# Optimization experiments

Hardware: AMD Instinct MI355X
Metric: run time of the kernel (lower is better)

Reference implementation:

```python
import jax, jax.numpy as jnp
import numpy as np

NF, EF, H, G, T, LAYERS = 133, 14, 300, 200, 12, 3
B, N_PER, PAIRS = 4096, 32, 32
N, E = B * N_PER, B * PAIRS * 2
R1, R2 = 550, 378  # readout dims per config defaults


def setup_inputs() -> dict:
    key = jax.random.key(0)
    ks = jax.random.split(key, 16)
    rng = np.random.default_rng(0)
    # edges within each graph, laid out as reverse pairs: 2i = (u->w), 2i+1 = (w->u)
    u = rng.integers(0, N_PER, size=(B, PAIRS))
    w = (u + 1 + rng.integers(0, N_PER - 1, size=(B, PAIRS))) % N_PER  # w != u
    offs = (np.arange(B) * N_PER)[:, None]
    u, w = u + offs, w + offs
    src = np.stack([u, w], axis=-1).reshape(-1).astype(np.int64)
    dst = np.stack([w, u], axis=-1).reshape(-1).astype(np.int64)
    node_graph = np.repeat(np.arange(B), N_PER).astype(np.int64)

    def lin(k, fin, fout):
        s = (2.0 / (fin + fout)) ** 0.5  # xavier_normal, gain=1
        return jax.random.normal(k, (fin, fout), jnp.float32) * s

    return {
        "v": jax.random.normal(ks[0], (N, NF + 1), jnp.float32),
        "e": jax.random.normal(ks[1], (E, EF + 1), jnp.float32),
        "globals_": jax.random.normal(ks[2], (B, G), jnp.float32),
        "Wi": lin(ks[3], NF + EF, H), "bi": jnp.zeros((H,), jnp.float32),
        "Wm": lin(ks[4], H, H), "bm": jnp.zeros((H,), jnp.float32),
        "Wa": lin(ks[5], NF + H, H), "ba": jnp.zeros((H,), jnp.float32),
        "Wr1": lin(ks[6], G + H, R1), "br1": jnp.zeros((R1,), jnp.float32),
        "Wr2": lin(ks[7], R1, R2), "br2": jnp.zeros((R2,), jnp.float32),
        "Wr3": lin(ks[8], R2, T), "br3": jnp.zeros((T,), jnp.float32),
        "src": jnp.asarray(src), "dst": jnp.asarray(dst),
        "node_graph": jnp.asarray(node_graph),
    }


def reference(v, e, globals_, Wi, bi, Wm, bm, Wa, ba,
              Wr1, br1, Wr2, br2, Wr3, br3, src, dst, node_graph):
    n = v.shape[0]
    b = globals_.shape[0]
    vv = v[:, :NF]          # strip trailing 'r' column
    ee = e[:, :EF]
    # edge init: h_0 = relu(W_i [src_v ; e])
    h0 = jax.nn.relu(jnp.concatenate([vv[src], ee], axis=1) @ Wi + bi)  # [E,H]
    rev = jnp.arange(h0.shape[0]) ^ 1  # reverse-pair edge layout
    h = h0
    for _ in range(LAYERS):
        # non-backtracking line-graph sum: incoming-to-src minus reverse edge
        acc = jax.ops.segment_sum(h, dst, num_segments=n)   # [N,H]
        m_e = acc[src] - h[rev]                             # [E,H]
        h = jax.nn.relu(h0 + m_e @ Wm + bm)                 # dropout p=0
    # reverse-graph copy_e sum => aggregate edges by ORIGINAL src node
    m_v = jax.ops.segment_sum(h, src, num_segments=n)       # [N,H]
    h_v = jax.nn.relu(jnp.concatenate([vv, m_v], axis=1) @ Wa + ba)
    # mean readout per graph
    cnt = jax.ops.segment_sum(jnp.ones((n,), v.dtype), node_graph, num_segments=b)
    out = jax.ops.segment_sum(h_v, node_graph, num_segments=b) / cnt[:, None]
    out = jax.nn.relu(jnp.concatenate([out, globals_], axis=1) @ Wr1 + br1)
    out = jax.nn.relu(out @ Wr2 + br2)
    return out @ Wr3 + br3
```

## Files before the change

### kernel.cpp

```cpp
#include <hip/hip_runtime.h>

typedef __bf16 bf16x8 __attribute__((ext_vector_type(8)));
typedef float f32x4 __attribute__((ext_vector_type(4)));
typedef unsigned short u16;
typedef unsigned int u32;
typedef unsigned long long u64;

#define NF_ 133
#define EF_ 14
#define HD 300
#define KH 320
#define K0 160
#define K2 448
#define NT 19
#define SHP 2432

__device__ __forceinline__ u16 f2bf(float f) {
    union { float f; u32 u; } v; v.f = f;
    u32 r = v.u + 0x7fffu + ((v.u >> 16) & 1u);
    return (u16)(r >> 16);
}
__device__ __forceinline__ float bf2f(u16 h) {
    union { u32 u; float f; } v; v.u = ((u32)h) << 16;
    return v.f;
}

__global__ void prep_w(const float* __restrict__ W, u16* __restrict__ Wt,
                       int K, int N, int KP, int NP, int gap) {
    int idx = blockIdx.x * 256 + threadIdx.x;
    if (idx >= NP * KP) return;
    int n = idx / KP, k = idx - n * KP;
    int kk = k;
    if (gap) kk = (k < 133) ? k : ((k >= 136 && k < 436) ? k - 3 : -1);
    float val = (kk >= 0 && kk < K && n < N) ? W[kk * N + n] : 0.f;
    Wt[idx] = f2bf(val);
}

__global__ void prep_glob(const float* __restrict__ glob, u16* __restrict__ Ar1) {
    int idx = blockIdx.x * 256 + threadIdx.x;
    if (idx >= 4096 * 212) return;
    int g = idx / 212, c = 300 + (idx - g * 212);
    float val = (c < 500) ? glob[g * 200 + (c - 300)] : 0.f;
    Ar1[g * 512 + c] = f2bf(val);
}

__global__ __launch_bounds__(512, 2) void gnn_mega(
    const float* __restrict__ vf, const float* __restrict__ ef,
    const int* __restrict__ src, const int* __restrict__ dst,
    const u16* __restrict__ WiT, const u16* __restrict__ WmT, const u16* __restrict__ WaT,
    const float* __restrict__ bi, const float* __restrict__ bm, const float* __restrict__ ba,
    u16* __restrict__ Ar1)
{
    __shared__ u16 sm[64 * KH];
    __shared__ u16 shT[8 * SHP];
    __shared__ u64 s_amask[32];
    __shared__ u64 s_smask[32];
    __shared__ int s_src[64];
    __shared__ unsigned char s_src8[64];

    const int g = blockIdx.x;
    const int tid = threadIdx.x;
    const int wave = tid >> 6;
    const int lane = tid & 63;
    const int lm = lane & 15;
    const int q = lane >> 4;

    if (tid < 64) {
        int sv = src[g * 64 + tid] - g * 32;
        int dv = dst[g * 64 + tid] - g * 32;
        s_src[tid] = sv;
        s_src8[tid] = (unsigned char)sv;
        #pragma unroll 1
        for (int n = 0; n < 32; ++n) {
            u64 bmA = __ballot(dv == n);
            u64 bmS = __ballot(sv == n);
            if (tid == 0) { s_amask[n] = bmA; s_smask[n] = bmS; }
        }
    }
    for (int i = tid; i < 9728; i += 512) ((u32*)shT)[i] = 0u;
    if (tid < 512) ((u32*)sm)[9728 + tid] = 0u;
    __syncthreads();

    for (int idx = tid; idx < 64 * K0; idx += 512) {
        int ed = idx / K0, c = idx - ed * K0;
        float val = 0.f;
        if (c < NF_) val = vf[(size_t)(g * 32 + s_src[ed]) * (NF_ + 1) + c];
        else if (c < NF_ + EF_) val = ef[(size_t)(g * 64 + ed) * (EF_ + 1) + (c - NF_)];
        sm[((c >> 3) << 9) + (ed << 3) + (c & 7)] = f2bf(val);
    }
    __syncthreads();

    u64 h0p[3][4];
    float bmv[3];
    {
        f32x4 acc[3][4];
        #pragma unroll
        for (int t = 0; t < 3; ++t)
            #pragma unroll
            for (int mt = 0; mt < 4; ++mt) acc[t][mt] = (f32x4){0.f, 0.f, 0.f, 0.f};
        #pragma unroll
        for (int ks = 0; ks < 5; ++ks) {
            bf16x8 af[4];
            #pragma unroll
            for (int mt = 0; mt < 4; ++mt)
                af[mt] = *(const bf16x8*)&sm[((ks * 4 + q) << 9) + ((mt * 16 + lm) << 3)];
            #pragma unroll
            for (int t = 0; t < 3; ++t) {
                int j = 8 * t + wave;
                if (j < NT) {
                    bf16x8 bfr = *(const bf16x8*)&WiT[(j * 16 + lm) * K0 + ks * 32 + q * 8];
                    #pragma unroll
                    for (int mt = 0; mt < 4; ++mt)
                        acc[t][mt] = __builtin_amdgcn_mfma_f32_16x16x32_bf16(af[mt], bfr, acc[t][mt], 0, 0, 0);
                }
            }
        }
        #pragma unroll
        for (int t = 0; t < 3; ++t) {
            int j = 8 * t + wave;
            int n = j * 16 + lm;
            bool ok = (j < NT) && (n < HD);
            float bv = ok ? bi[n] : 0.f;
            bmv[t] = ok ? bm[n] : 0.f;
            #pragma unroll
            for (int mt = 0; mt < 4; ++mt) {
                u64 w = 0;
                #pragma unroll
                for (int r = 0; r < 4; ++r) {
                    float hv = acc[t][mt][r] + bv;
                    hv = hv > 0.f ? hv : 0.f;
                    w |= ((u64)f2bf(hv)) << (16 * r);
                }
                h0p[t][mt] = w;
                if (ok) *(u64*)&shT[(mt * 2 + (q >> 1)) * SHP + n * 8 + (q & 1) * 4] = w;
            }
        }
    }

    for (int layer = 0; layer < 3; ++layer) {
        __syncthreads();
        {
            u64 am[4];
            #pragma unroll
            for (int mt = 0; mt < 4; ++mt) {
                int e = mt * 16 + lm;
                am[mt] = s_amask[s_src8[e]] & ~(1ull << (e ^ 1));
            }
            bf16x8 bfrag[2][4];
            #pragma unroll
            for (int ks = 0; ks < 2; ++ks) {
                int kb = ks * 32 + q * 8;
                #pragma unroll
                for (int mt = 0; mt < 4; ++mt) {
                    union { u32 w[4]; bf16x8 v; } fb;
                    #pragma unroll
                    for (int jj = 0; jj < 4; ++jj) {
                        u32 lo = (u32)((am[mt] >> (kb + 2 * jj)) & 1ull) * 0x3F80u;
                        u32 hi = (u32)((am[mt] >> (kb + 2 * jj + 1)) & 1ull) * 0x3F80u;
                        fb.w[jj] = lo | (hi << 16);
                    }
                    bfrag[ks][mt] = fb.v;
                }
            }
            #pragma unroll
            for (int t = 0; t < 3; ++t) {
                int j = 8 * t + wave;
                if (j < NT) {
                    f32x4 mac[4];
                    #pragma unroll
                    for (int mt = 0; mt < 4; ++mt) mac[mt] = (f32x4){0.f, 0.f, 0.f, 0.f};
                    #pragma unroll
                    for (int ks = 0; ks < 2; ++ks) {
                        bf16x8 af = *(const bf16x8*)&shT[(ks * 4 + q) * SHP + (j * 16 + lm) * 8];
                        #pragma unroll
                        for (int mt = 0; mt < 4; ++mt)
                            mac[mt] = __builtin_amdgcn_mfma_f32_16x16x32_bf16(af, bfrag[ks][mt], mac[mt], 0, 0, 0);
                    }
                    #pragma unroll
                    for (int mt = 0; mt < 4; ++mt) {
                        u64 w = 0;
                        #pragma unroll
                        for (int r = 0; r < 4; ++r) w |= ((u64)f2bf(mac[mt][r])) << (16 * r);
                        *(u64*)&sm[(j * 2 + (q >> 1)) * 512 + (mt * 16 + lm) * 8 + (q & 1) * 4] = w;
                    }
                }
            }
        }
        __syncthreads();
        {
            f32x4 acc[3][4];
            #pragma unroll
            for (int t = 0; t < 3; ++t)
                #pragma unroll
                for (int mt = 0; mt < 4; ++mt) acc[t][mt] = (f32x4){0.f, 0.f, 0.f, 0.f};
            #pragma unroll
            for (int ks = 0; ks < 10; ++ks) {
                bf16x8 af[4];
                #pragma unroll
                for (int mt = 0; mt < 4; ++mt)
                    af[mt] = *(const bf16x8*)&sm[((ks * 4 + q) << 9) + ((mt * 16 + lm) << 3)];
                #pragma unroll
                for (int t = 0; t < 3; ++t) {
                    int j = 8 * t + wave;
                    if (j < NT) {
                        bf16x8 bfr = *(const bf16x8*)&WmT[(j * 16 + lm) * KH + ks * 32 + q * 8];
                        #pragma unroll
                        for (int mt = 0; mt < 4; ++mt)
                            acc[t][mt] = __builtin_amdgcn_mfma_f32_16x16x32_bf16(af[mt], bfr, acc[t][mt], 0, 0, 0);
                    }
                }
            }
            #pragma unroll
            for (int t = 0; t < 3; ++t) {
                int j = 8 * t + wave;
                int n = j * 16 + lm;
                bool ok = (j < NT) && (n < HD);
                #pragma unroll
                for (int mt = 0; mt < 4; ++mt) {
                    u64 w = 0;
                    #pragma unroll
                    for (int r = 0; r < 4; ++r) {
                        float h0v = bf2f((u16)(h0p[t][mt] >> (16 * r)));
                        float hv = h0v + acc[t][mt][r] + bmv[t];
                        hv = hv > 0.f ? hv : 0.f;
                        w |= ((u64)f2bf(hv)) << (16 * r);
                    }
                    if (ok) *(u64*)&shT[(mt * 2 + (q >> 1)) * SHP + n * 8 + (q & 1) * 4] = w;
                }
            }
        }
    }
    __syncthreads();

    for (int idx = tid; idx < 32 * K2; idx += 512) {
        int n = idx / K2, c = idx - n * K2;
        float val = (c < NF_) ? vf[(size_t)(g * 32 + n) * (NF_ + 1) + c] : 0.f;
        sm[((c >> 3) << 8) + (n << 3) + (c & 7)] = f2bf(val);
    }
    __syncthreads();

    {
        bf16x8 sfrag[2][2];
        #pragma unroll
        for (int ks = 0; ks < 2; ++ks) {
            int kb = ks * 32 + q * 8;
            #pragma unroll
            for (int mt = 0; mt < 2; ++mt) {
                u64 msk = s_smask[mt * 16 + lm];
                union { u32 w[4]; bf16x8 v; } fb;
                #pragma unroll
                for (int jj = 0; jj < 4; ++jj) {
                    u32 lo = (u32)((msk >> (kb + 2 * jj)) & 1ull) * 0x3F80u;
                    u32 hi = (u32)((msk >> (kb + 2 * jj + 1)) & 1ull) * 0x3F80u;
                    fb.w[jj] = lo | (hi << 16);
                }
                sfrag[ks][mt] = fb.v;
            }
        }
        #pragma unroll
        for (int t = 0; t < 3; ++t) {
            int j = 8 * t + wave;
            if (j < NT) {
                f32x4 vacc[2];
                #pragma unroll
                for (int mt = 0; mt < 2; ++mt) vacc[mt] = (f32x4){0.f, 0.f, 0.f, 0.f};
                #pragma unroll
                for (int ks = 0; ks < 2; ++ks) {
                    bf16x8 af = *(const bf16x8*)&shT[(ks * 4 + q) * SHP + (j * 16 + lm) * 8];
                    #pragma unroll
                    for (int mt = 0; mt < 2; ++mt)
                        vacc[mt] = __builtin_amdgcn_mfma_f32_16x16x32_bf16(af, sfrag[ks][mt], vacc[mt], 0, 0, 0);
                }
                #pragma unroll
                for (int mt = 0; mt < 2; ++mt) {
                    u64 w = 0;
                    #pragma unroll
                    for (int r = 0; r < 4; ++r) w |= ((u64)f2bf(vacc[mt][r])) << (16 * r);
                    *(u64*)&sm[(17 + j * 2 + (q >> 1)) * 256 + (mt * 16 + lm) * 8 + (q & 1) * 4] = w;
                }
            }
        }
    }
    __syncthreads();

    {
        f32x4 acc2[3][2];
        #pragma unroll
        for (int t = 0; t < 3; ++t)
            #pragma unroll
            for (int mt = 0; mt < 2; ++mt) acc2[t][mt] = (f32x4){0.f, 0.f, 0.f, 0.f};
        #pragma unroll
        for (int ks = 0; ks < 14; ++ks) {
            bf16x8 af[2];
            #pragma unroll
            for (int mt = 0; mt < 2; ++mt)
                af[mt] = *(const bf16x8*)&sm[((ks * 4 + q) << 8) + ((mt * 16 + lm) << 3)];
            #pragma unroll
            for (int t = 0; t < 3; ++t) {
                int j = 8 * t + wave;
                if (j < NT) {
                    bf16x8 bfr = *(const bf16x8*)&WaT[(j * 16 + lm) * K2 + ks * 32 + q * 8];
                    #pragma unroll
                    for (int mt = 0; mt < 2; ++mt)
                        acc2[t][mt] = __builtin_amdgcn_mfma_f32_16x16x32_bf16(af[mt], bfr, acc2[t][mt], 0, 0, 0);
                }
            }
        }
        #pragma unroll
        for (int t = 0; t < 3; ++t) {
            int j = 8 * t + wave;
            int n = j * 16 + lm;
            bool ok = (j < NT) && (n < HD);
            float bav = ok ? ba[n] : 0.f;
            float s = 0.f;
            #pragma unroll
            for (int mt = 0; mt < 2; ++mt)
                #pragma unroll
                for (int r = 0; r < 4; ++r) {
                    float hv = acc2[t][mt][r] + bav;
                    s += (hv > 0.f ? hv : 0.f);
                }
            s += __shfl_xor(s, 16);
            s += __shfl_xor(s, 32);
            if (ok && q == 0) Ar1[g * 512 + n] = f2bf(s * 0.03125f);
        }
    }
}

template<int RELU, int OUTBF16>
__global__ __launch_bounds__(256, 4) void gemm_ro(
    const u16* __restrict__ A, const u16* __restrict__ Bt, const float* __restrict__ bias,
    const int KP, const int Nreal, const int outPitch, void* __restrict__ outp, const int nsteps)
{
    const int tid = threadIdx.x;
    const int wv = tid >> 6, lane = tid & 63, lm = lane & 15, q = lane >> 4;
    const int row0 = blockIdx.x * 64;
    const int col = blockIdx.y * 64 + wv * 16 + lm;
    f32x4 acc[4];
    #pragma unroll
    for (int mt = 0; mt < 4; ++mt) acc[mt] = (f32x4){0.f, 0.f, 0.f, 0.f};
    const u16* bp = Bt + col * KP + q * 8;
    const u16* ap = A + (row0 + lm) * KP + q * 8;
    for (int ks = 0; ks < nsteps; ++ks) {
        bf16x8 bfr = *(const bf16x8*)(bp + ks * 32);
        #pragma unroll
        for (int mt = 0; mt < 4; ++mt) {
            bf16x8 afr = *(const bf16x8*)(ap + mt * 16 * KP + ks * 32);
            acc[mt] = __builtin_amdgcn_mfma_f32_16x16x32_bf16(afr, bfr, acc[mt], 0, 0, 0);
        }
    }
    const float bv = (col < Nreal) ? bias[col] : 0.f;
    #pragma unroll
    for (int mt = 0; mt < 4; ++mt) {
        #pragma unroll
        for (int r = 0; r < 4; ++r) {
            int row = row0 + mt * 16 + q * 4 + r;
            float val = acc[mt][r] + bv;
            if (RELU) val = val > 0.f ? val : 0.f;
            if (OUTBF16) {
                ((u16*)outp)[row * outPitch + col] = (col < Nreal) ? f2bf(val) : (u16)0;
            } else {
                if (col < Nreal) ((float*)outp)[row * outPitch + col] = val;
            }
        }
    }
}

extern "C" void kernel_launch(void* const* d_in, const int* in_sizes, int n_in,
                              void* d_out, int out_size, void* d_ws, size_t ws_size,
                              hipStream_t stream) {
    (void)in_sizes; (void)n_in; (void)out_size; (void)ws_size;
    const float* v   = (const float*)d_in[0];
    const float* e   = (const float*)d_in[1];
    const float* glb = (const float*)d_in[2];
    const float* Wi  = (const float*)d_in[3];
    const float* bi  = (const float*)d_in[4];
    const float* Wm  = (const float*)d_in[5];
    const float* bm  = (const float*)d_in[6];
    const float* Wa  = (const float*)d_in[7];
    const float* ba  = (const float*)d_in[8];
    const float* Wr1 = (const float*)d_in[9];
    const float* br1 = (const float*)d_in[10];
    const float* Wr2 = (const float*)d_in[11];
    const float* br2 = (const float*)d_in[12];
    const float* Wr3 = (const float*)d_in[13];
    const float* br3 = (const float*)d_in[14];
    const int* src = (const int*)d_in[15];
    const int* dst = (const int*)d_in[16];

    char* ws = (char*)d_ws;
    u16* WiT  = (u16*)(ws + 0);
    u16* WmT  = (u16*)(ws + 97280);
    u16* WaT  = (u16*)(ws + 291840);
    u16* Wr1T = (u16*)(ws + 564224);
    u16* Wr2T = (u16*)(ws + 1154048);
    u16* Wr3T = (u16*)(ws + 1596416);
    u16* Ar1  = (u16*)(ws + 1645568);
    u16* Ar2  = (u16*)(ws + 5839872);
    u16* Ar3  = (u16*)(ws + 10558464);

    prep_w<<<190,  256, 0, stream>>>(Wi,  WiT,  147, 300, 160, 304, 0);
    prep_w<<<380,  256, 0, stream>>>(Wm,  WmT,  300, 300, 320, 304, 0);
    prep_w<<<532,  256, 0, stream>>>(Wa,  WaT,  433, 300, 448, 304, 1);
    prep_w<<<1152, 256, 0, stream>>>(Wr1, Wr1T, 500, 550, 512, 576, 0);
    prep_w<<<864,  256, 0, stream>>>(Wr2, Wr2T, 550, 378, 576, 384, 0);
    prep_w<<<96,   256, 0, stream>>>(Wr3, Wr3T, 378, 12,  384, 64,  0);
    prep_glob<<<3392, 256, 0, stream>>>(glb, Ar1);

    gnn_mega<<<4096, 512, 0, stream>>>(v, e, src, dst, WiT, WmT, WaT, bi, bm, ba, Ar1);

    gemm_ro<1, 1><<<dim3(64, 9), 256, 0, stream>>>(Ar1, Wr1T, br1, 512, 550, 576, Ar2, 16);
    gemm_ro<1, 1><<<dim3(64, 6), 256, 0, stream>>>(Ar2, Wr2T, br2, 576, 378, 384, Ar3, 18);
    gemm_ro<0, 0><<<dim3(64, 1), 256, 0, stream>>>(Ar3, Wr3T, br3, 384, 12, 12, d_out, 12);
}
```

Measured before the change: 1.001 ms.

## Shrink gnn_mega blocks to 4 waves with 5 column tiles per wave

```diff
diff --git a/kernel.cpp b/kernel.cpp
--- a/kernel.cpp
+++ b/kernel.cpp
@@ -44,7 +44,7 @@
     Ar1[g * 512 + c] = f2bf(val);
 }
 
-__global__ __launch_bounds__(512, 2) void gnn_mega(
+__global__ __launch_bounds__(256, 2) void gnn_mega(
     const float* __restrict__ vf, const float* __restrict__ ef,
     const int* __restrict__ src, const int* __restrict__ dst,
     const u16* __restrict__ WiT, const u16* __restrict__ WmT, const u16* __restrict__ WaT,
@@ -77,11 +77,14 @@
             if (tid == 0) { s_amask[n] = bmA; s_smask[n] = bmS; }
         }
     }
-    for (int i = tid; i < 9728; i += 512) ((u32*)shT)[i] = 0u;
-    if (tid < 512) ((u32*)sm)[9728 + tid] = 0u;
+    if (tid < 128) {
+        int kr = tid >> 4, c = 300 + ((tid >> 2) & 3), w = tid & 3;
+        ((u32*)shT)[kr * 1216 + c * 4 + w] = 0u;
+    }
+    for (int i = tid; i < 512; i += 256) ((u32*)sm)[9728 + i] = 0u;
     __syncthreads();
 
-    for (int idx = tid; idx < 64 * K0; idx += 512) {
+    for (int idx = tid; idx < 64 * K0; idx += 256) {
         int ed = idx / K0, c = idx - ed * K0;
         float val = 0.f;
         if (c < NF_) val = vf[(size_t)(g * 32 + s_src[ed]) * (NF_ + 1) + c];
@@ -90,12 +93,11 @@
     }
     __syncthreads();
 
-    u64 h0p[3][4];
-    float bmv[3];
+    u64 h0p[5][4];
     {
-        f32x4 acc[3][4];
-        #pragma unroll
-        for (int t = 0; t < 3; ++t)
+        f32x4 acc[5][4];
+        #pragma unroll
+        for (int t = 0; t < 5; ++t)
             #pragma unroll
             for (int mt = 0; mt < 4; ++mt) acc[t][mt] = (f32x4){0.f, 0.f, 0.f, 0.f};
         #pragma unroll
@@ -105,8 +107,8 @@
             for (int mt = 0; mt < 4; ++mt)
                 af[mt] = *(const bf16x8*)&sm[((ks * 4 + q) << 9) + ((mt * 16 + lm) << 3)];
             #pragma unroll
-            for (int t = 0; t < 3; ++t) {
-                int j = 8 * t + wave;
+            for (int t = 0; t < 5; ++t) {
+                int j = t * 4 + wave;
                 if (j < NT) {
                     bf16x8 bfr = *(const bf16x8*)&WiT[(j * 16 + lm) * K0 + ks * 32 + q * 8];
                     #pragma unroll
@@ -116,22 +118,23 @@
             }
         }
         #pragma unroll
-        for (int t = 0; t < 3; ++t) {
-            int j = 8 * t + wave;
+        for (int t = 0; t < 5; ++t) {
+            int j = t * 4 + wave;
             int n = j * 16 + lm;
             bool ok = (j < NT) && (n < HD);
             float bv = ok ? bi[n] : 0.f;
-            bmv[t] = ok ? bm[n] : 0.f;
+            float bmval = ok ? bm[n] : 0.f;
             #pragma unroll
             for (int mt = 0; mt < 4; ++mt) {
-                u64 w = 0;
+                u64 w = 0, wr = 0;
                 #pragma unroll
                 for (int r = 0; r < 4; ++r) {
                     float hv = acc[t][mt][r] + bv;
                     hv = hv > 0.f ? hv : 0.f;
-                    w |= ((u64)f2bf(hv)) << (16 * r);
-                }
-                h0p[t][mt] = w;
+                    w  |= ((u64)f2bf(hv)) << (16 * r);
+                    wr |= ((u64)f2bf(hv + bmval)) << (16 * r);
+                }
+                h0p[t][mt] = wr;
                 if (ok) *(u64*)&shT[(mt * 2 + (q >> 1)) * SHP + n * 8 + (q & 1) * 4] = w;
             }
         }
@@ -140,31 +143,27 @@
     for (int layer = 0; layer < 3; ++layer) {
         __syncthreads();
         {
-            u64 am[4];
-            #pragma unroll
-            for (int mt = 0; mt < 4; ++mt) {
-                int e = mt * 16 + lm;
-                am[mt] = s_amask[s_src8[e]] & ~(1ull << (e ^ 1));
-            }
             bf16x8 bfrag[2][4];
             #pragma unroll
             for (int ks = 0; ks < 2; ++ks) {
                 int kb = ks * 32 + q * 8;
                 #pragma unroll
                 for (int mt = 0; mt < 4; ++mt) {
+                    int e = mt * 16 + lm;
+                    u64 am = s_amask[s_src8[e]] & ~(1ull << (e ^ 1));
                     union { u32 w[4]; bf16x8 v; } fb;
                     #pragma unroll
                     for (int jj = 0; jj < 4; ++jj) {
-                        u32 lo = (u32)((am[mt] >> (kb + 2 * jj)) & 1ull) * 0x3F80u;
-                        u32 hi = (u32)((am[mt] >> (kb + 2 * jj + 1)) & 1ull) * 0x3F80u;
+                        u32 lo = (u32)((am >> (kb + 2 * jj)) & 1ull) * 0x3F80u;
+                        u32 hi = (u32)((am >> (kb + 2 * jj + 1)) & 1ull) * 0x3F80u;
                         fb.w[jj] = lo | (hi << 16);
                     }
                     bfrag[ks][mt] = fb.v;
                 }
             }
             #pragma unroll
-            for (int t = 0; t < 3; ++t) {
-                int j = 8 * t + wave;
+            for (int t = 0; t < 5; ++t) {
+                int j = t * 4 + wave;
                 if (j < NT) {
                     f32x4 mac[4];
                     #pragma unroll
@@ -188,9 +187,9 @@
         }
         __syncthreads();
         {
-            f32x4 acc[3][4];
-            #pragma unroll
-            for (int t = 0; t < 3; ++t)
+            f32x4 acc[5][4];
+            #pragma unroll
+            for (int t = 0; t < 5; ++t)
                 #pragma unroll
                 for (int mt = 0; mt < 4; ++mt) acc[t][mt] = (f32x4){0.f, 0.f, 0.f, 0.f};
             #pragma unroll
@@ -200,8 +199,8 @@
                 for (int mt = 0; mt < 4; ++mt)
                     af[mt] = *(const bf16x8*)&sm[((ks * 4 + q) << 9) + ((mt * 16 + lm) << 3)];
                 #pragma unroll
-                for (int t = 0; t < 3; ++t) {
-                    int j = 8 * t + wave;
+                for (int t = 0; t < 5; ++t) {
+                    int j = t * 4 + wave;
                     if (j < NT) {
                         bf16x8 bfr = *(const bf16x8*)&WmT[(j * 16 + lm) * KH + ks * 32 + q * 8];
                         #pragma unroll
@@ -211,8 +210,8 @@
                 }
             }
             #pragma unroll
-            for (int t = 0; t < 3; ++t) {
-                int j = 8 * t + wave;
+            for (int t = 0; t < 5; ++t) {
+                int j = t * 4 + wave;
                 int n = j * 16 + lm;
                 bool ok = (j < NT) && (n < HD);
                 #pragma unroll
@@ -221,7 +220,7 @@
                     #pragma unroll
                     for (int r = 0; r < 4; ++r) {
                         float h0v = bf2f((u16)(h0p[t][mt] >> (16 * r)));
-                        float hv = h0v + acc[t][mt][r] + bmv[t];
+                        float hv = h0v + acc[t][mt][r];
                         hv = hv > 0.f ? hv : 0.f;
                         w |= ((u64)f2bf(hv)) << (16 * r);
                     }
@@ -232,7 +231,7 @@
     }
     __syncthreads();
 
-    for (int idx = tid; idx < 32 * K2; idx += 512) {
+    for (int idx = tid; idx < 32 * K2; idx += 256) {
         int n = idx / K2, c = idx - n * K2;
         float val = (c < NF_) ? vf[(size_t)(g * 32 + n) * (NF_ + 1) + c] : 0.f;
         sm[((c >> 3) << 8) + (n << 3) + (c & 7)] = f2bf(val);
@@ -258,8 +257,8 @@
             }
         }
         #pragma unroll
-        for (int t = 0; t < 3; ++t) {
-            int j = 8 * t + wave;
+        for (int t = 0; t < 5; ++t) {
+            int j = t * 4 + wave;
             if (j < NT) {
                 f32x4 vacc[2];
                 #pragma unroll
@@ -284,9 +283,9 @@
     __syncthreads();
 
     {
-        f32x4 acc2[3][2];
-        #pragma unroll
-        for (int t = 0; t < 3; ++t)
+        f32x4 acc2[5][2];
+        #pragma unroll
+        for (int t = 0; t < 5; ++t)
             #pragma unroll
             for (int mt = 0; mt < 2; ++mt) acc2[t][mt] = (f32x4){0.f, 0.f, 0.f, 0.f};
         #pragma unroll
@@ -296,8 +295,8 @@
             for (int mt = 0; mt < 2; ++mt)
                 af[mt] = *(const bf16x8*)&sm[((ks * 4 + q) << 8) + ((mt * 16 + lm) << 3)];
             #pragma unroll
-            for (int t = 0; t < 3; ++t) {
-                int j = 8 * t + wave;
+            for (int t = 0; t < 5; ++t) {
+                int j = t * 4 + wave;
                 if (j < NT) {
                     bf16x8 bfr = *(const bf16x8*)&WaT[(j * 16 + lm) * K2 + ks * 32 + q * 8];
                     #pragma unroll
@@ -307,8 +306,8 @@
             }
         }
         #pragma unroll
-        for (int t = 0; t < 3; ++t) {
-            int j = 8 * t + wave;
+        for (int t = 0; t < 5; ++t) {
+            int j = t * 4 + wave;
             int n = j * 16 + lm;
             bool ok = (j < NT) && (n < HD);
             float bav = ok ? ba[n] : 0.f;
@@ -407,7 +406,7 @@
     prep_w<<<96,   256, 0, stream>>>(Wr3, Wr3T, 378, 12,  384, 64,  0);
     prep_glob<<<3392, 256, 0, stream>>>(glb, Ar1);
 
-    gnn_mega<<<4096, 512, 0, stream>>>(v, e, src, dst, WiT, WmT, WaT, bi, bm, ba, Ar1);
+    gnn_mega<<<4096, 256, 0, stream>>>(v, e, src, dst, WiT, WmT, WaT, bi, bm, ba, Ar1);
 
     gemm_ro<1, 1><<<dim3(64, 9), 256, 0, stream>>>(Ar1, Wr1T, br1, 512, 550, 576, Ar2, 16);
     gemm_ro<1, 1><<<dim3(64, 6), 256, 0, stream>>>(Ar2, Wr2T, br2, 576, 378, 384, Ar3, 18);
```

New measurement: 1.042 ms. 4.1% more time.

## Batch-load weight and activation fragments into registers and fold bias into h0

Applied to the files above, without the earlier changes.

```diff
diff --git a/kernel.cpp b/kernel.cpp
--- a/kernel.cpp
+++ b/kernel.cpp
@@ -44,7 +44,7 @@
     Ar1[g * 512 + c] = f2bf(val);
 }
 
-__global__ __launch_bounds__(512, 2) void gnn_mega(
+__global__ __launch_bounds__(512, 1) void gnn_mega(
     const float* __restrict__ vf, const float* __restrict__ ef,
     const int* __restrict__ src, const int* __restrict__ dst,
     const u16* __restrict__ WiT, const u16* __restrict__ WmT, const u16* __restrict__ WaT,
@@ -77,7 +77,10 @@
             if (tid == 0) { s_amask[n] = bmA; s_smask[n] = bmS; }
         }
     }
-    for (int i = tid; i < 9728; i += 512) ((u32*)shT)[i] = 0u;
+    if (tid < 128) {
+        int kr = tid >> 4, c = 300 + ((tid >> 2) & 3), w = tid & 3;
+        ((u32*)shT)[kr * 1216 + c * 4 + w] = 0u;
+    }
     if (tid < 512) ((u32*)sm)[9728 + tid] = 0u;
     __syncthreads();
 
@@ -90,48 +93,57 @@
     }
     __syncthreads();
 
+    const int j0 = wave, j1 = 8 + wave, j2 = 16 + wave;
+    const bool ok2 = (j2 < NT);
+    const int n0 = j0 * 16 + lm, n1 = j1 * 16 + lm, n2 = j2 * 16 + lm;
+
     u64 h0p[3][4];
-    float bmv[3];
     {
+        bf16x8 af[5][4];
+        #pragma unroll
+        for (int ks = 0; ks < 5; ++ks)
+            #pragma unroll
+            for (int mt = 0; mt < 4; ++mt)
+                af[ks][mt] = *(const bf16x8*)&sm[((ks * 4 + q) << 9) + ((mt * 16 + lm) << 3)];
+        bf16x8 wf[5][3];
+        #pragma unroll
+        for (int ks = 0; ks < 5; ++ks) {
+            wf[ks][0] = *(const bf16x8*)&WiT[n0 * K0 + ks * 32 + q * 8];
+            wf[ks][1] = *(const bf16x8*)&WiT[n1 * K0 + ks * 32 + q * 8];
+            if (ok2) wf[ks][2] = *(const bf16x8*)&WiT[n2 * K0 + ks * 32 + q * 8];
+        }
         f32x4 acc[3][4];
         #pragma unroll
         for (int t = 0; t < 3; ++t)
             #pragma unroll
             for (int mt = 0; mt < 4; ++mt) acc[t][mt] = (f32x4){0.f, 0.f, 0.f, 0.f};
         #pragma unroll
-        for (int ks = 0; ks < 5; ++ks) {
-            bf16x8 af[4];
-            #pragma unroll
-            for (int mt = 0; mt < 4; ++mt)
-                af[mt] = *(const bf16x8*)&sm[((ks * 4 + q) << 9) + ((mt * 16 + lm) << 3)];
+        for (int ks = 0; ks < 5; ++ks)
             #pragma unroll
             for (int t = 0; t < 3; ++t) {
-                int j = 8 * t + wave;
-                if (j < NT) {
-                    bf16x8 bfr = *(const bf16x8*)&WiT[(j * 16 + lm) * K0 + ks * 32 + q * 8];
-                    #pragma unroll
-                    for (int mt = 0; mt < 4; ++mt)
-                        acc[t][mt] = __builtin_amdgcn_mfma_f32_16x16x32_bf16(af[mt], bfr, acc[t][mt], 0, 0, 0);
-                }
-            }
-        }
+                if (t == 2 && !ok2) continue;
+                #pragma unroll
+                for (int mt = 0; mt < 4; ++mt)
+                    acc[t][mt] = __builtin_amdgcn_mfma_f32_16x16x32_bf16(af[ks][mt], wf[ks][t], acc[t][mt], 0, 0, 0);
+            }
         #pragma unroll
         for (int t = 0; t < 3; ++t) {
-            int j = 8 * t + wave;
+            int j = t * 8 + wave;
             int n = j * 16 + lm;
             bool ok = (j < NT) && (n < HD);
             float bv = ok ? bi[n] : 0.f;
-            bmv[t] = ok ? bm[n] : 0.f;
+            float bmval = ok ? bm[n] : 0.f;
             #pragma unroll
             for (int mt = 0; mt < 4; ++mt) {
-                u64 w = 0;
+                u64 w = 0, wr = 0;
                 #pragma unroll
                 for (int r = 0; r < 4; ++r) {
                     float hv = acc[t][mt][r] + bv;
                     hv = hv > 0.f ? hv : 0.f;
-                    w |= ((u64)f2bf(hv)) << (16 * r);
-                }
-                h0p[t][mt] = w;
+                    w  |= ((u64)f2bf(hv)) << (16 * r);
+                    wr |= ((u64)f2bf(hv + bmval)) << (16 * r);
+                }
+                h0p[t][mt] = wr;
                 if (ok) *(u64*)&shT[(mt * 2 + (q >> 1)) * SHP + n * 8 + (q & 1) * 4] = w;
             }
         }
@@ -139,12 +151,20 @@
 
     for (int layer = 0; layer < 3; ++layer) {
         __syncthreads();
+        bf16x8 wA[5][3];
+        #pragma unroll
+        for (int ks = 0; ks < 5; ++ks) {
+            wA[ks][0] = *(const bf16x8*)&WmT[n0 * KH + ks * 32 + q * 8];
+            wA[ks][1] = *(const bf16x8*)&WmT[n1 * KH + ks * 32 + q * 8];
+            if (ok2) wA[ks][2] = *(const bf16x8*)&WmT[n2 * KH + ks * 32 + q * 8];
+        }
         {
-            u64 am[4];
-            #pragma unroll
-            for (int mt = 0; mt < 4; ++mt) {
-                int e = mt * 16 + lm;
-                am[mt] = s_amask[s_src8[e]] & ~(1ull << (e ^ 1));
+            bf16x8 af1[2][3];
+            #pragma unroll
+            for (int ks = 0; ks < 2; ++ks) {
+                af1[ks][0] = *(const bf16x8*)&shT[(ks * 4 + q) * SHP + (j0 * 16 + lm) * 8];
+                af1[ks][1] = *(const bf16x8*)&shT[(ks * 4 + q) * SHP + (j1 * 16 + lm) * 8];
+                if (ok2) af1[ks][2] = *(const bf16x8*)&shT[(ks * 4 + q) * SHP + (j2 * 16 + lm) * 8];
             }
             bf16x8 bfrag[2][4];
             #pragma unroll
@@ -152,11 +172,13 @@
                 int kb = ks * 32 + q * 8;
                 #pragma unroll
                 for (int mt = 0; mt < 4; ++mt) {
+                    int e = mt * 16 + lm;
+                    u64 am = s_amask[s_src8[e]] & ~(1ull << (e ^ 1));
                     union { u32 w[4]; bf16x8 v; } fb;
                     #pragma unroll
                     for (int jj = 0; jj < 4; ++jj) {
-                        u32 lo = (u32)((am[mt] >> (kb + 2 * jj)) & 1ull) * 0x3F80u;
-                        u32 hi = (u32)((am[mt] >> (kb + 2 * jj + 1)) & 1ull) * 0x3F80u;
+                        u32 lo = (u32)((am >> (kb + 2 * jj)) & 1ull) * 0x3F80u;
+                        u32 hi = (u32)((am >> (kb + 2 * jj + 1)) & 1ull) * 0x3F80u;
                         fb.w[jj] = lo | (hi << 16);
                     }
                     bfrag[ks][mt] = fb.v;
@@ -164,25 +186,22 @@
             }
             #pragma unroll
             for (int t = 0; t < 3; ++t) {
-                int j = 8 * t + wave;
-                if (j < NT) {
-                    f32x4 mac[4];
-                    #pragma unroll
-                    for (int mt = 0; mt < 4; ++mt) mac[mt] = (f32x4){0.f, 0.f, 0.f, 0.f};
-                    #pragma unroll
-                    for (int ks = 0; ks < 2; ++ks) {
-                        bf16x8 af = *(const bf16x8*)&shT[(ks * 4 + q) * SHP + (j * 16 + lm) * 8];
-                        #pragma unroll
-                        for (int mt = 0; mt < 4; ++mt)
-                            mac[mt] = __builtin_amdgcn_mfma_f32_16x16x32_bf16(af, bfrag[ks][mt], mac[mt], 0, 0, 0);
-                    }
-                    #pragma unroll
-                    for (int mt = 0; mt < 4; ++mt) {
-                        u64 w = 0;
-                        #pragma unroll
-                        for (int r = 0; r < 4; ++r) w |= ((u64)f2bf(mac[mt][r])) << (16 * r);
-                        *(u64*)&sm[(j * 2 + (q >> 1)) * 512 + (mt * 16 + lm) * 8 + (q & 1) * 4] = w;
-                    }
+                if (t == 2 && !ok2) continue;
+                int j = t * 8 + wave;
+                f32x4 mac[4];
+                #pragma unroll
+                for (int mt = 0; mt < 4; ++mt) mac[mt] = (f32x4){0.f, 0.f, 0.f, 0.f};
+                #pragma unroll
+                for (int ks = 0; ks < 2; ++ks)
+                    #pragma unroll
+                    for (int mt = 0; mt < 4; ++mt)
+                        mac[mt] = __builtin_amdgcn_mfma_f32_16x16x32_bf16(af1[ks][t], bfrag[ks][mt], mac[mt], 0, 0, 0);
+                #pragma unroll
+                for (int mt = 0; mt < 4; ++mt) {
+                    u64 w = 0;
+                    #pragma unroll
+                    for (int r = 0; r < 4; ++r) w |= ((u64)f2bf(mac[mt][r])) << (16 * r);
+                    *(u64*)&sm[(j * 2 + (q >> 1)) * 512 + (mt * 16 + lm) * 8 + (q & 1) * 4] = w;
                 }
             }
         }
@@ -193,26 +212,50 @@
             for (int t = 0; t < 3; ++t)
                 #pragma unroll
                 for (int mt = 0; mt < 4; ++mt) acc[t][mt] = (f32x4){0.f, 0.f, 0.f, 0.f};
-            #pragma unroll
-            for (int ks = 0; ks < 10; ++ks) {
-                bf16x8 af[4];
-                #pragma unroll
-                for (int mt = 0; mt < 4; ++mt)
-                    af[mt] = *(const bf16x8*)&sm[((ks * 4 + q) << 9) + ((mt * 16 + lm) << 3)];
-                #pragma unroll
-                for (int t = 0; t < 3; ++t) {
-                    int j = 8 * t + wave;
-                    if (j < NT) {
-                        bf16x8 bfr = *(const bf16x8*)&WmT[(j * 16 + lm) * KH + ks * 32 + q * 8];
+            {
+                bf16x8 afA[5][4];
+                #pragma unroll
+                for (int ks = 0; ks < 5; ++ks)
+                    #pragma unroll
+                    for (int mt = 0; mt < 4; ++mt)
+                        afA[ks][mt] = *(const bf16x8*)&sm[((ks * 4 + q) << 9) + ((mt * 16 + lm) << 3)];
+                #pragma unroll
+                for (int ks = 0; ks < 5; ++ks)
+                    #pragma unroll
+                    for (int t = 0; t < 3; ++t) {
+                        if (t == 2 && !ok2) continue;
                         #pragma unroll
                         for (int mt = 0; mt < 4; ++mt)
-                            acc[t][mt] = __builtin_amdgcn_mfma_f32_16x16x32_bf16(af[mt], bfr, acc[t][mt], 0, 0, 0);
+                            acc[t][mt] = __builtin_amdgcn_mfma_f32_16x16x32_bf16(afA[ks][mt], wA[ks][t], acc[t][mt], 0, 0, 0);
                     }
-                }
+            }
+            {
+                bf16x8 wB[5][3];
+                #pragma unroll
+                for (int ks = 0; ks < 5; ++ks) {
+                    wB[ks][0] = *(const bf16x8*)&WmT[n0 * KH + (ks + 5) * 32 + q * 8];
+                    wB[ks][1] = *(const bf16x8*)&WmT[n1 * KH + (ks + 5) * 32 + q * 8];
+                    if (ok2) wB[ks][2] = *(const bf16x8*)&WmT[n2 * KH + (ks + 5) * 32 + q * 8];
+                }
+                bf16x8 afB[5][4];
+                #pragma unroll
+                for (int ks = 0; ks < 5; ++ks)
+                    #pragma unroll
+                    for (int mt = 0; mt < 4; ++mt)
+                        afB[ks][mt] = *(const bf16x8*)&sm[(((ks + 5) * 4 + q) << 9) + ((mt * 16 + lm) << 3)];
+                #pragma unroll
+                for (int ks = 0; ks < 5; ++ks)
+                    #pragma unroll
+                    for (int t = 0; t < 3; ++t) {
+                        if (t == 2 && !ok2) continue;
+                        #pragma unroll
+                        for (int mt = 0; mt < 4; ++mt)
+                            acc[t][mt] = __builtin_amdgcn_mfma_f32_16x16x32_bf16(afB[ks][mt], wB[ks][t], acc[t][mt], 0, 0, 0);
+                    }
             }
             #pragma unroll
             for (int t = 0; t < 3; ++t) {
-                int j = 8 * t + wave;
+                int j = t * 8 + wave;
                 int n = j * 16 + lm;
                 bool ok = (j < NT) && (n < HD);
                 #pragma unroll
@@ -220,8 +263,7 @@
                     u64 w = 0;
                     #pragma unroll
                     for (int r = 0; r < 4; ++r) {
-                        float h0v = bf2f((u16)(h0p[t][mt] >> (16 * r)));
-                        float hv = h0v + acc[t][mt][r] + bmv[t];
+                        float hv = bf2f((u16)(h0p[t][mt] >> (16 * r))) + acc[t][mt][r];
                         hv = hv > 0.f ? hv : 0.f;
                         w |= ((u64)f2bf(hv)) << (16 * r);
                     }
@@ -232,14 +274,23 @@
     }
     __syncthreads();
 
-    for (int idx = tid; idx < 32 * K2; idx += 512) {
-        int n = idx / K2, c = idx - n * K2;
+    for (int idx = tid; idx < 32 * 136; idx += 512) {
+        int n = idx / 136, c = idx - n * 136;
         float val = (c < NF_) ? vf[(size_t)(g * 32 + n) * (NF_ + 1) + c] : 0.f;
         sm[((c >> 3) << 8) + (n << 3) + (c & 7)] = f2bf(val);
     }
-    __syncthreads();
-
+    if (tid < 256) {
+        int n = tid >> 3, c = 440 + (tid & 7);
+        sm[((c >> 3) << 8) + (n << 3) + (c & 7)] = (u16)0;
+    }
     {
+        bf16x8 af1[2][3];
+        #pragma unroll
+        for (int ks = 0; ks < 2; ++ks) {
+            af1[ks][0] = *(const bf16x8*)&shT[(ks * 4 + q) * SHP + (j0 * 16 + lm) * 8];
+            af1[ks][1] = *(const bf16x8*)&shT[(ks * 4 + q) * SHP + (j1 * 16 + lm) * 8];
+            if (ok2) af1[ks][2] = *(const bf16x8*)&shT[(ks * 4 + q) * SHP + (j2 * 16 + lm) * 8];
+        }
         bf16x8 sfrag[2][2];
         #pragma unroll
         for (int ks = 0; ks < 2; ++ks) {
@@ -259,25 +310,22 @@
         }
         #pragma unroll
         for (int t = 0; t < 3; ++t) {
-            int j = 8 * t + wave;
-            if (j < NT) {
-                f32x4 vacc[2];
-                #pragma unroll
-                for (int mt = 0; mt < 2; ++mt) vacc[mt] = (f32x4){0.f, 0.f, 0.f, 0.f};
-                #pragma unroll
-                for (int ks = 0; ks < 2; ++ks) {
-                    bf16x8 af = *(const bf16x8*)&shT[(ks * 4 + q) * SHP + (j * 16 + lm) * 8];
-                    #pragma unroll
-                    for (int mt = 0; mt < 2; ++mt)
-                        vacc[mt] = __builtin_amdgcn_mfma_f32_16x16x32_bf16(af, sfrag[ks][mt], vacc[mt], 0, 0, 0);
-                }
-                #pragma unroll
-                for (int mt = 0; mt < 2; ++mt) {
-                    u64 w = 0;
-                    #pragma unroll
-                    for (int r = 0; r < 4; ++r) w |= ((u64)f2bf(vacc[mt][r])) << (16 * r);
-                    *(u64*)&sm[(17 + j * 2 + (q >> 1)) * 256 + (mt * 16 + lm) * 8 + (q & 1) * 4] = w;
-                }
+            if (t == 2 && !ok2) continue;
+            int j = t * 8 + wave;
+            f32x4 vacc[2];
+            #pragma unroll
+            for (int mt = 0; mt < 2; ++mt) vacc[mt] = (f32x4){0.f, 0.f, 0.f, 0.f};
+            #pragma unroll
+            for (int ks = 0; ks < 2; ++ks)
+                #pragma unroll
+                for (int mt = 0; mt < 2; ++mt)
+                    vacc[mt] = __builtin_amdgcn_mfma_f32_16x16x32_bf16(af1[ks][t], sfrag[ks][mt], vacc[mt], 0, 0, 0);
+            #pragma unroll
+            for (int mt = 0; mt < 2; ++mt) {
+                u64 w = 0;
+                #pragma unroll
+                for (int r = 0; r < 4; ++r) w |= ((u64)f2bf(vacc[mt][r])) << (16 * r);
+                *(u64*)&sm[(17 + j * 2 + (q >> 1)) * 256 + (mt * 16 + lm) * 8 + (q & 1) * 4] = w;
             }
         }
     }
@@ -290,25 +338,34 @@
             #pragma unroll
             for (int mt = 0; mt < 2; ++mt) acc2[t][mt] = (f32x4){0.f, 0.f, 0.f, 0.f};
         #pragma unroll
-        for (int ks = 0; ks < 14; ++ks) {
-            bf16x8 af[2];
-            #pragma unroll
-            for (int mt = 0; mt < 2; ++mt)
-                af[mt] = *(const bf16x8*)&sm[((ks * 4 + q) << 8) + ((mt * 16 + lm) << 3)];
-            #pragma unroll
-            for (int t = 0; t < 3; ++t) {
-                int j = 8 * t + wave;
-                if (j < NT) {
-                    bf16x8 bfr = *(const bf16x8*)&WaT[(j * 16 + lm) * K2 + ks * 32 + q * 8];
+        for (int half = 0; half < 2; ++half) {
+            const int kbase = half * 7;
+            bf16x8 af[7][2];
+            #pragma unroll
+            for (int ks = 0; ks < 7; ++ks)
+                #pragma unroll
+                for (int mt = 0; mt < 2; ++mt)
+                    af[ks][mt] = *(const bf16x8*)&sm[(((kbase + ks) * 4 + q) << 8) + ((mt * 16 + lm) << 3)];
+            bf16x8 wf[7][3];
+            #pragma unroll
+            for (int ks = 0; ks < 7; ++ks) {
+                wf[ks][0] = *(const bf16x8*)&WaT[n0 * K2 + (kbase + ks) * 32 + q * 8];
+                wf[ks][1] = *(const bf16x8*)&WaT[n1 * K2 + (kbase + ks) * 32 + q * 8];
+                if (ok2) wf[ks][2] = *(const bf16x8*)&WaT[n2 * K2 + (kbase + ks) * 32 + q * 8];
+            }
+            #pragma unroll
+            for (int ks = 0; ks < 7; ++ks)
+                #pragma unroll
+                for (int t = 0; t < 3; ++t) {
+                    if (t == 2 && !ok2) continue;
                     #pragma unroll
                     for (int mt = 0; mt < 2; ++mt)
-                        acc2[t][mt] = __builtin_amdgcn_mfma_f32_16x16x32_bf16(af[mt], bfr, acc2[t][mt], 0, 0, 0);
-                }
-            }
+                        acc2[t][mt] = __builtin_amdgcn_mfma_f32_16x16x32_bf16(af[ks][mt], wf[ks][t], acc2[t][mt], 0, 0, 0);
+                }
         }
         #pragma unroll
         for (int t = 0; t < 3; ++t) {
-            int j = 8 * t + wave;
+            int j = t * 8 + wave;
             int n = j * 16 + lm;
             bool ok = (j < NT) && (n < HD);
             float bav = ok ? ba[n] : 0.f;
```

Result: slower. 1.818 ms (+81.6%).
